# Performance work log

Hardware: AMD Instinct MI355X
Metric: run time of the kernel (lower is better)

## Reference

```python
import jax, jax.numpy as jnp
import numpy as np

INPUT_LAYER_SIZE = 40960 * 2
LAYER1_SIZE = 512
LAYER2_SIZE = 32
LAYER3_SIZE = 32
BATCH = 4096


def setup_inputs() -> dict:
    key = jax.random.key(0)
    ks = jax.random.split(key, 10)
    # Sparse one-hot style features: mostly zeros with ~30 active entries per side.
    def sparse_features(k, n_active=30):
        kidx, = jax.random.split(k, 1)
        idx = jax.random.randint(kidx, (BATCH, n_active), 0, 40960)
        feats = jnp.zeros((BATCH, 40960), dtype=jnp.float32)
        return feats.at[jnp.arange(BATCH)[:, None], idx].set(1.0)
    w_features = sparse_features(ks[0])
    b_features = sparse_features(ks[1])
    s_in = 1.0 / np.sqrt(INPUT_LAYER_SIZE)
    s1 = 1.0 / np.sqrt(LAYER1_SIZE)
    s2 = 1.0 / np.sqrt(LAYER2_SIZE)
    s3 = 1.0 / np.sqrt(LAYER3_SIZE)
    return {
        "w_features": w_features,
        "b_features": b_features,
        "W_in": jax.random.uniform(ks[2], (LAYER1_SIZE, INPUT_LAYER_SIZE), jnp.float32, -s_in, s_in),
        "b_in": jax.random.uniform(ks[3], (LAYER1_SIZE,), jnp.float32, -s_in, s_in),
        "W1": jax.random.uniform(ks[4], (LAYER2_SIZE, LAYER1_SIZE), jnp.float32, -s1, s1),
        "b1": jax.random.uniform(ks[5], (LAYER2_SIZE,), jnp.float32, -s1, s1),
        "W2": jax.random.uniform(ks[6], (LAYER3_SIZE, LAYER2_SIZE), jnp.float32, -s2, s2),
        "b2": jax.random.uniform(ks[7], (LAYER3_SIZE,), jnp.float32, -s2, s2),
        "W3": jax.random.uniform(ks[8], (1, LAYER3_SIZE), jnp.float32, -s3, s3),
        "b3": jax.random.uniform(ks[9], (1,), jnp.float32, -s3, s3),
    }


def reference(w_features, b_features, W_in, b_in, W1, b1, W2, b2, W3, b3):
    # Concatenate both perspectives: [B, 81920]
    x = jnp.concatenate([w_features, b_features], axis=1)
    # Huge sparse-input accumulator layer (the kernel-headroom op)
    accum = x @ W_in.T + b_in                       # [B, 512]
    l1 = jnp.clip(accum, 0.0, 1.0)                  # clipped ReLU
    l2 = jnp.clip(l1 @ W1.T + b1, 0.0, 1.0)         # [B, 32]
    l3 = jnp.clip(l2 @ W2.T + b2, 0.0, 1.0)         # [B, 32]
    return l3 @ W3.T + b3                           # [B, 1]
```

## Files before the change

kernel.cpp:

```cpp
#include <hip/hip_runtime.h>
#include <hip/hip_bf16.h>

#define IN_PER_SIDE   40960
#define IN_TOTAL      81920
#define L1            512
#define L2            32
#define L3_           32
#define BATCH         4096
#define MAXIDX        128

typedef float v4f __attribute__((ext_vector_type(4)));

#define WT_BYTES   ((size_t)IN_TOTAL * L1 * sizeof(float))
#define CNT_BYTES  ((size_t)BATCH * sizeof(int))
#define IDX_BYTES  ((size_t)BATCH * MAXIDX * sizeof(int))

__global__ __launch_bounds__(256) void stream_prep(
    const float* __restrict__ W, float* __restrict__ WT,
    const float* __restrict__ wf, const float* __restrict__ bfeat,
    int* __restrict__ cnt, int* __restrict__ idxs)
{
    __shared__ float tile[64][65];
    const int cls = blockIdx.x % 9;

    if (cls < 5) {
        const int tindex = (blockIdx.x / 9) * 5 + cls;
        const int jt = (tindex % 1280) * 64;
        const int ot = (tindex / 1280) * 64;
        const int tx = threadIdx.x & 15;
        const int ty = threadIdx.x >> 4;

#pragma unroll
        for (int k = 0; k < 4; ++k) {
            const int o = ty + 16 * k;
            const v4f* p = (const v4f*)&W[(size_t)(ot + o) * IN_TOTAL + jt + 4 * tx];
            v4f v = __builtin_nontemporal_load(p);
            tile[4 * tx + 0][o] = v.x;
            tile[4 * tx + 1][o] = v.y;
            tile[4 * tx + 2][o] = v.z;
            tile[4 * tx + 3][o] = v.w;
        }
        __syncthreads();
#pragma unroll
        for (int k = 0; k < 4; ++k) {
            const int j = ty + 16 * k;
            v4f v;
            v.x = tile[j][4 * tx + 0];
            v.y = tile[j][4 * tx + 1];
            v.z = tile[j][4 * tx + 2];
            v.w = tile[j][4 * tx + 3];
            *(v4f*)&WT[(size_t)(jt + j) * L1 + ot + 4 * tx] = v;
        }
    } else {
        const int sindex = (blockIdx.x / 9) * 4 + (cls - 5);
        const int row  = sindex >> 1;
        const int side = sindex & 1;
        const float* src = side ? bfeat : wf;
        const int    bias = side ? IN_PER_SIDE : 0;
        const v4f* p = (const v4f*)(src + (size_t)row * IN_PER_SIDE);
        int* ic = cnt + row;
        int* il = idxs + (size_t)row * MAXIDX;

        const int nvec = IN_PER_SIDE / 4;
        for (int i = threadIdx.x; i < nvec; i += 256) {
            v4f v = __builtin_nontemporal_load(p + i);
            if (v.x != 0.0f) il[atomicAdd(ic, 1)] = bias + 4 * i + 0;
            if (v.y != 0.0f) il[atomicAdd(ic, 1)] = bias + 4 * i + 1;
            if (v.z != 0.0f) il[atomicAdd(ic, 1)] = bias + 4 * i + 2;
            if (v.w != 0.0f) il[atomicAdd(ic, 1)] = bias + 4 * i + 3;
        }
    }
}

__global__ __launch_bounds__(512) void gather_mlp(
    const float* __restrict__ WT,
    const int* __restrict__ cnt, const int* __restrict__ idxs,
    const float* __restrict__ b_in,
    const float* __restrict__ W1, const float* __restrict__ b1,
    const float* __restrict__ W2, const float* __restrict__ b2,
    const float* __restrict__ W3, const float* __restrict__ b3,
    float* __restrict__ out)
{
    const int b = blockIdx.x;
    const int t = threadIdx.x;

    __shared__ int   sidx[MAXIDX];
    __shared__ float l1s[L1];
    __shared__ float l2acc[L2];
    __shared__ float l2s[L2];
    __shared__ float l3s[L3_];

    const int n = cnt[b];
    if (t < n) sidx[t] = idxs[(size_t)b * MAXIDX + t];
    const float bias_t = b_in[t];
    __syncthreads();

    float a0 = 0.0f, a1 = 0.0f, a2 = 0.0f, a3 = 0.0f;
    int i = 0;
    for (; i + 8 <= n; i += 8) {
        const float v0 = WT[(size_t)sidx[i + 0] * L1 + t];
        const float v1 = WT[(size_t)sidx[i + 1] * L1 + t];
        const float v2 = WT[(size_t)sidx[i + 2] * L1 + t];
        const float v3 = WT[(size_t)sidx[i + 3] * L1 + t];
        const float v4 = WT[(size_t)sidx[i + 4] * L1 + t];
        const float v5 = WT[(size_t)sidx[i + 5] * L1 + t];
        const float v6 = WT[(size_t)sidx[i + 6] * L1 + t];
        const float v7 = WT[(size_t)sidx[i + 7] * L1 + t];
        a0 += v0; a1 += v1; a2 += v2; a3 += v3;
        a0 += v4; a1 += v5; a2 += v6; a3 += v7;
    }
    for (; i < n; ++i) a0 += WT[(size_t)sidx[i] * L1 + t];

    float acc = bias_t + ((a0 + a1) + (a2 + a3));
    l1s[t] = fminf(fmaxf(acc, 0.0f), 1.0f);
    __syncthreads();

    {
        const int k = t >> 4;
        const int g = t & 15;
        const float* w = W1 + (size_t)k * L1;
        float p = 0.0f;
        for (int o = g; o < L1; o += 16) p += w[o] * l1s[o];
#pragma unroll
        for (int off = 8; off > 0; off >>= 1) p += __shfl_down(p, off, 16);
        if (g == 0) l2acc[k] = p;
    }
    __syncthreads();
    if (t < L2) l2s[t] = fminf(fmaxf(l2acc[t] + b1[t], 0.0f), 1.0f);
    __syncthreads();

    if (t < L3_) {
        const float* w = W2 + (size_t)t * L2;
        float p = b2[t];
#pragma unroll
        for (int q = 0; q < L2; ++q) p += w[q] * l2s[q];
        l3s[t] = fminf(fmaxf(p, 0.0f), 1.0f);
    }
    __syncthreads();

    if (t == 0) {
        float p = b3[0];
#pragma unroll
        for (int q = 0; q < L3_; ++q) p += W3[q] * l3s[q];
        out[b] = p;
    }
}

__global__ __launch_bounds__(512) void nnue_fallback(
    const float* __restrict__ wf, const float* __restrict__ bfeat,
    const float* __restrict__ W_in, const float* __restrict__ b_in,
    const float* __restrict__ W1, const float* __restrict__ b1,
    const float* __restrict__ W2, const float* __restrict__ b2,
    const float* __restrict__ W3, const float* __restrict__ b3,
    float* __restrict__ out)
{
    const int b = blockIdx.x;
    const int t = threadIdx.x;
    __shared__ int   idxs[MAXIDX];
    __shared__ int   scnt;
    __shared__ float l1s[L1];
    __shared__ float l2acc[L2];
    __shared__ float l2s[L2];
    __shared__ float l3s[L3_];

    if (t == 0) scnt = 0;
    __syncthreads();
    const v4f* wrow = (const v4f*)(wf    + (size_t)b * IN_PER_SIDE);
    const v4f* brow = (const v4f*)(bfeat + (size_t)b * IN_PER_SIDE);
    for (int i = t; i < IN_PER_SIDE / 4; i += 512) {
        v4f v = wrow[i];
        if (v.x != 0.0f) idxs[atomicAdd(&scnt, 1)] = 4 * i + 0;
        if (v.y != 0.0f) idxs[atomicAdd(&scnt, 1)] = 4 * i + 1;
        if (v.z != 0.0f) idxs[atomicAdd(&scnt, 1)] = 4 * i + 2;
        if (v.w != 0.0f) idxs[atomicAdd(&scnt, 1)] = 4 * i + 3;
        v4f u = brow[i];
        if (u.x != 0.0f) idxs[atomicAdd(&scnt, 1)] = IN_PER_SIDE + 4 * i + 0;
        if (u.y != 0.0f) idxs[atomicAdd(&scnt, 1)] = IN_PER_SIDE + 4 * i + 1;
        if (u.z != 0.0f) idxs[atomicAdd(&scnt, 1)] = IN_PER_SIDE + 4 * i + 2;
        if (u.w != 0.0f) idxs[atomicAdd(&scnt, 1)] = IN_PER_SIDE + 4 * i + 3;
    }
    __syncthreads();
    const int n = scnt;
    float a0 = 0.0f;
    const float* wr = W_in + (size_t)t;
    const float* row = W_in + (size_t)t * IN_TOTAL;
    for (int i = 0; i < n; ++i) a0 += row[idxs[i]];
    l1s[t] = fminf(fmaxf(b_in[t] + a0, 0.0f), 1.0f);
    __syncthreads();
    {
        const int k = t >> 4, g = t & 15;
        const float* w = W1 + (size_t)k * L1;
        float p = 0.0f;
        for (int o = g; o < L1; o += 16) p += w[o] * l1s[o];
#pragma unroll
        for (int off = 8; off > 0; off >>= 1) p += __shfl_down(p, off, 16);
        if (g == 0) l2acc[k] = p;
    }
    __syncthreads();
    if (t < L2) l2s[t] = fminf(fmaxf(l2acc[t] + b1[t], 0.0f), 1.0f);
    __syncthreads();
    if (t < L3_) {
        const float* w = W2 + (size_t)t * L2;
        float p = b2[t];
#pragma unroll
        for (int q = 0; q < L2; ++q) p += w[q] * l2s[q];
        l3s[t] = fminf(fmaxf(p, 0.0f), 1.0f);
    }
    __syncthreads();
    if (t == 0) {
        float p = b3[0];
#pragma unroll
        for (int q = 0; q < L3_; ++q) p += W3[q] * l3s[q];
        out[b] = p;
    }
}

extern "C" void kernel_launch(void* const* d_in, const int* in_sizes, int n_in,
                              void* d_out, int out_size, void* d_ws, size_t ws_size,
                              hipStream_t stream) {
    const float* wf   = (const float*)d_in[0];
    const float* bfeat= (const float*)d_in[1];
    const float* W_in = (const float*)d_in[2];
    const float* b_in = (const float*)d_in[3];
    const float* W1   = (const float*)d_in[4];
    const float* b1   = (const float*)d_in[5];
    const float* W2   = (const float*)d_in[6];
    const float* b2   = (const float*)d_in[7];
    const float* W3   = (const float*)d_in[8];
    const float* b3   = (const float*)d_in[9];
    float* out = (float*)d_out;

    const size_t need = WT_BYTES + CNT_BYTES + IDX_BYTES;
    if (ws_size >= need) {
        float* WT  = (float*)d_ws;
        int*   cnt = (int*)((char*)d_ws + WT_BYTES);
        int*   idx = (int*)((char*)d_ws + WT_BYTES + CNT_BYTES);

        hipMemsetAsync(cnt, 0, CNT_BYTES, stream);

        stream_prep<<<18432, 256, 0, stream>>>(W_in, WT, wf, bfeat, cnt, idx);
        gather_mlp<<<BATCH, 512, 0, stream>>>(WT, cnt, idx, b_in,
                                              W1, b1, W2, b2, W3, b3, out);
    } else {
        nnue_fallback<<<BATCH, 512, 0, stream>>>(
            wf, bfeat, W_in, b_in, W1, b1, W2, b2, W3, b3, out);
    }
}
```

Measured before the change: 1.454 ms.

## Fuse sparse index extraction into gather kernel and store transposed weights in fp16

Moves the dense-feature scan into the per-batch gather/MLP kernel, collecting active indices in shared memory instead of global arrays with a memset. The transposed input weight matrix is now stored in half precision, and each block gathers 16-byte half vectors across 8 waves, then reduces partial sums in shared memory. This cuts transpose write traffic, gather traffic and one launch. In exchange it adds fp16 rounding of the weights and serialises the scan with the gather per block.

```diff
diff --git a/kernel.cpp b/kernel.cpp
--- a/kernel.cpp
+++ b/kernel.cpp
@@ -9,72 +9,49 @@
 #define BATCH         4096
 #define MAXIDX        128
 
-typedef float v4f __attribute__((ext_vector_type(4)));
-
-#define WT_BYTES   ((size_t)IN_TOTAL * L1 * sizeof(float))
-#define CNT_BYTES  ((size_t)BATCH * sizeof(int))
-#define IDX_BYTES  ((size_t)BATCH * MAXIDX * sizeof(int))
-
-__global__ __launch_bounds__(256) void stream_prep(
-    const float* __restrict__ W, float* __restrict__ WT,
-    const float* __restrict__ wf, const float* __restrict__ bfeat,
-    int* __restrict__ cnt, int* __restrict__ idxs)
+typedef float    v4f __attribute__((ext_vector_type(4)));
+typedef float    v8f __attribute__((ext_vector_type(8)));
+typedef _Float16 v4h __attribute__((ext_vector_type(4)));
+typedef _Float16 v8h __attribute__((ext_vector_type(8)));
+
+#define WT_BYTES ((size_t)IN_TOTAL * L1 * sizeof(_Float16))
+
+__global__ __launch_bounds__(256) void transpose_win(
+    const float* __restrict__ W, _Float16* __restrict__ WTh)
 {
     __shared__ float tile[64][65];
-    const int cls = blockIdx.x % 9;
-
-    if (cls < 5) {
-        const int tindex = (blockIdx.x / 9) * 5 + cls;
-        const int jt = (tindex % 1280) * 64;
-        const int ot = (tindex / 1280) * 64;
-        const int tx = threadIdx.x & 15;
-        const int ty = threadIdx.x >> 4;
-
-#pragma unroll
-        for (int k = 0; k < 4; ++k) {
-            const int o = ty + 16 * k;
-            const v4f* p = (const v4f*)&W[(size_t)(ot + o) * IN_TOTAL + jt + 4 * tx];
-            v4f v = __builtin_nontemporal_load(p);
-            tile[4 * tx + 0][o] = v.x;
-            tile[4 * tx + 1][o] = v.y;
-            tile[4 * tx + 2][o] = v.z;
-            tile[4 * tx + 3][o] = v.w;
-        }
-        __syncthreads();
-#pragma unroll
-        for (int k = 0; k < 4; ++k) {
-            const int j = ty + 16 * k;
-            v4f v;
-            v.x = tile[j][4 * tx + 0];
-            v.y = tile[j][4 * tx + 1];
-            v.z = tile[j][4 * tx + 2];
-            v.w = tile[j][4 * tx + 3];
-            *(v4f*)&WT[(size_t)(jt + j) * L1 + ot + 4 * tx] = v;
-        }
-    } else {
-        const int sindex = (blockIdx.x / 9) * 4 + (cls - 5);
-        const int row  = sindex >> 1;
-        const int side = sindex & 1;
-        const float* src = side ? bfeat : wf;
-        const int    bias = side ? IN_PER_SIDE : 0;
-        const v4f* p = (const v4f*)(src + (size_t)row * IN_PER_SIDE);
-        int* ic = cnt + row;
-        int* il = idxs + (size_t)row * MAXIDX;
-
-        const int nvec = IN_PER_SIDE / 4;
-        for (int i = threadIdx.x; i < nvec; i += 256) {
-            v4f v = __builtin_nontemporal_load(p + i);
-            if (v.x != 0.0f) il[atomicAdd(ic, 1)] = bias + 4 * i + 0;
-            if (v.y != 0.0f) il[atomicAdd(ic, 1)] = bias + 4 * i + 1;
-            if (v.z != 0.0f) il[atomicAdd(ic, 1)] = bias + 4 * i + 2;
-            if (v.w != 0.0f) il[atomicAdd(ic, 1)] = bias + 4 * i + 3;
-        }
-    }
-}
-
-__global__ __launch_bounds__(512) void gather_mlp(
-    const float* __restrict__ WT,
-    const int* __restrict__ cnt, const int* __restrict__ idxs,
+    const int jt = blockIdx.x * 64;
+    const int ot = blockIdx.y * 64;
+    const int tx = threadIdx.x & 15;
+    const int ty = threadIdx.x >> 4;
+
+#pragma unroll
+    for (int k = 0; k < 4; ++k) {
+        const int o = ty + 16 * k;
+        const v4f* p = (const v4f*)&W[(size_t)(ot + o) * IN_TOTAL + jt + 4 * tx];
+        v4f v = __builtin_nontemporal_load(p);
+        tile[4 * tx + 0][o] = v.x;
+        tile[4 * tx + 1][o] = v.y;
+        tile[4 * tx + 2][o] = v.z;
+        tile[4 * tx + 3][o] = v.w;
+    }
+    __syncthreads();
+#pragma unroll
+    for (int k = 0; k < 4; ++k) {
+        const int j = ty + 16 * k;
+        v4f v;
+        v.x = tile[j][4 * tx + 0];
+        v.y = tile[j][4 * tx + 1];
+        v.z = tile[j][4 * tx + 2];
+        v.w = tile[j][4 * tx + 3];
+        v4h h = __builtin_convertvector(v, v4h);
+        *(v4h*)&WTh[(size_t)(jt + j) * L1 + ot + 4 * tx] = h;
+    }
+}
+
+__global__ __launch_bounds__(512) void nnue_fused(
+    const float* __restrict__ wf, const float* __restrict__ bfeat,
+    const _Float16* __restrict__ WTh,
     const float* __restrict__ b_in,
     const float* __restrict__ W1, const float* __restrict__ b1,
     const float* __restrict__ W2, const float* __restrict__ b2,
@@ -85,55 +62,91 @@
     const int t = threadIdx.x;
 
     __shared__ int   sidx[MAXIDX];
+    __shared__ int   scnt;
+    __shared__ float accs[8 * 64 * 9];
     __shared__ float l1s[L1];
     __shared__ float l2acc[L2];
     __shared__ float l2s[L2];
     __shared__ float l3s[L3_];
 
-    const int n = cnt[b];
-    if (t < n) sidx[t] = idxs[(size_t)b * MAXIDX + t];
-    const float bias_t = b_in[t];
-    __syncthreads();
-
-    float a0 = 0.0f, a1 = 0.0f, a2 = 0.0f, a3 = 0.0f;
-    int i = 0;
-    for (; i + 8 <= n; i += 8) {
-        const float v0 = WT[(size_t)sidx[i + 0] * L1 + t];
-        const float v1 = WT[(size_t)sidx[i + 1] * L1 + t];
-        const float v2 = WT[(size_t)sidx[i + 2] * L1 + t];
-        const float v3 = WT[(size_t)sidx[i + 3] * L1 + t];
-        const float v4 = WT[(size_t)sidx[i + 4] * L1 + t];
-        const float v5 = WT[(size_t)sidx[i + 5] * L1 + t];
-        const float v6 = WT[(size_t)sidx[i + 6] * L1 + t];
-        const float v7 = WT[(size_t)sidx[i + 7] * L1 + t];
-        a0 += v0; a1 += v1; a2 += v2; a3 += v3;
-        a0 += v4; a1 += v5; a2 += v6; a3 += v7;
-    }
-    for (; i < n; ++i) a0 += WT[(size_t)sidx[i] * L1 + t];
-
-    float acc = bias_t + ((a0 + a1) + (a2 + a3));
-    l1s[t] = fminf(fmaxf(acc, 0.0f), 1.0f);
-    __syncthreads();
-
-    {
-        const int k = t >> 4;
-        const int g = t & 15;
-        const float* w = W1 + (size_t)k * L1;
+    if (t == 0) scnt = 0;
+    __syncthreads();
+
+    const v4f* wrow = (const v4f*)(wf    + (size_t)b * IN_PER_SIDE);
+    const v4f* brow = (const v4f*)(bfeat + (size_t)b * IN_PER_SIDE);
+    const int nvec = IN_PER_SIDE / 4;
+
+    for (int i = t; i < nvec; i += 512) {
+        v4f v = __builtin_nontemporal_load(wrow + i);
+        if (v.x + v.y + v.z + v.w != 0.0f) {
+            if (v.x != 0.0f) sidx[atomicAdd(&scnt, 1)] = 4 * i + 0;
+            if (v.y != 0.0f) sidx[atomicAdd(&scnt, 1)] = 4 * i + 1;
+            if (v.z != 0.0f) sidx[atomicAdd(&scnt, 1)] = 4 * i + 2;
+            if (v.w != 0.0f) sidx[atomicAdd(&scnt, 1)] = 4 * i + 3;
+        }
+        v4f u = __builtin_nontemporal_load(brow + i);
+        if (u.x + u.y + u.z + u.w != 0.0f) {
+            if (u.x != 0.0f) sidx[atomicAdd(&scnt, 1)] = IN_PER_SIDE + 4 * i + 0;
+            if (u.y != 0.0f) sidx[atomicAdd(&scnt, 1)] = IN_PER_SIDE + 4 * i + 1;
+            if (u.z != 0.0f) sidx[atomicAdd(&scnt, 1)] = IN_PER_SIDE + 4 * i + 2;
+            if (u.w != 0.0f) sidx[atomicAdd(&scnt, 1)] = IN_PER_SIDE + 4 * i + 3;
+        }
+    }
+    __syncthreads();
+
+    const int n = scnt;
+    const int w = t >> 6;
+    const int l = t & 63;
+    const v8h* WTH8 = (const v8h*)WTh;
+
+    v8f acc0 = {0,0,0,0,0,0,0,0};
+    v8f acc1 = {0,0,0,0,0,0,0,0};
+    int k = w;
+    for (; k + 16 <= n; k += 16) {
+        v8h h0 = WTH8[(size_t)sidx[k]     * 64 + l];
+        v8h h1 = WTH8[(size_t)sidx[k + 8] * 64 + l];
+        acc0 += __builtin_convertvector(h0, v8f);
+        acc1 += __builtin_convertvector(h1, v8f);
+    }
+    for (; k < n; k += 8)
+        acc0 += __builtin_convertvector(WTH8[(size_t)sidx[k] * 64 + l], v8f);
+    acc0 += acc1;
+
+    {
+        float* dst = &accs[(w * 64 + l) * 9];
+#pragma unroll
+        for (int i = 0; i < 8; ++i) dst[i] = acc0[i];
+    }
+    __syncthreads();
+
+    {
+        const int ll = t >> 3, c = t & 7;
+        float s = 0.0f;
+#pragma unroll
+        for (int ww = 0; ww < 8; ++ww) s += accs[(ww * 64 + ll) * 9 + c];
+        l1s[t] = fminf(fmaxf(s + b_in[t], 0.0f), 1.0f);
+    }
+    __syncthreads();
+
+    {
+        const int kk = t >> 4;
+        const int gg = t & 15;
+        const float* wp = W1 + (size_t)kk * L1;
         float p = 0.0f;
-        for (int o = g; o < L1; o += 16) p += w[o] * l1s[o];
+        for (int o = gg; o < L1; o += 16) p += wp[o] * l1s[o];
 #pragma unroll
         for (int off = 8; off > 0; off >>= 1) p += __shfl_down(p, off, 16);
-        if (g == 0) l2acc[k] = p;
+        if (gg == 0) l2acc[kk] = p;
     }
     __syncthreads();
     if (t < L2) l2s[t] = fminf(fmaxf(l2acc[t] + b1[t], 0.0f), 1.0f);
     __syncthreads();
 
     if (t < L3_) {
-        const float* w = W2 + (size_t)t * L2;
+        const float* wp = W2 + (size_t)t * L2;
         float p = b2[t];
 #pragma unroll
-        for (int q = 0; q < L2; ++q) p += w[q] * l2s[q];
+        for (int q = 0; q < L2; ++q) p += wp[q] * l2s[q];
         l3s[t] = fminf(fmaxf(p, 0.0f), 1.0f);
     }
     __syncthreads();
@@ -182,16 +195,15 @@
     __syncthreads();
     const int n = scnt;
     float a0 = 0.0f;
-    const float* wr = W_in + (size_t)t;
     const float* row = W_in + (size_t)t * IN_TOTAL;
     for (int i = 0; i < n; ++i) a0 += row[idxs[i]];
     l1s[t] = fminf(fmaxf(b_in[t] + a0, 0.0f), 1.0f);
     __syncthreads();
     {
         const int k = t >> 4, g = t & 15;
-        const float* w = W1 + (size_t)k * L1;
+        const float* wp = W1 + (size_t)k * L1;
         float p = 0.0f;
-        for (int o = g; o < L1; o += 16) p += w[o] * l1s[o];
+        for (int o = g; o < L1; o += 16) p += wp[o] * l1s[o];
 #pragma unroll
         for (int off = 8; off > 0; off >>= 1) p += __shfl_down(p, off, 16);
         if (g == 0) l2acc[k] = p;
@@ -200,10 +212,10 @@
     if (t < L2) l2s[t] = fminf(fmaxf(l2acc[t] + b1[t], 0.0f), 1.0f);
     __syncthreads();
     if (t < L3_) {
-        const float* w = W2 + (size_t)t * L2;
+        const float* wp = W2 + (size_t)t * L2;
         float p = b2[t];
 #pragma unroll
-        for (int q = 0; q < L2; ++q) p += w[q] * l2s[q];
+        for (int q = 0; q < L2; ++q) p += wp[q] * l2s[q];
         l3s[t] = fminf(fmaxf(p, 0.0f), 1.0f);
     }
     __syncthreads();
@@ -230,17 +242,12 @@
     const float* b3   = (const float*)d_in[9];
     float* out = (float*)d_out;
 
-    const size_t need = WT_BYTES + CNT_BYTES + IDX_BYTES;
-    if (ws_size >= need) {
-        float* WT  = (float*)d_ws;
-        int*   cnt = (int*)((char*)d_ws + WT_BYTES);
-        int*   idx = (int*)((char*)d_ws + WT_BYTES + CNT_BYTES);
-
-        hipMemsetAsync(cnt, 0, CNT_BYTES, stream);
-
-        stream_prep<<<18432, 256, 0, stream>>>(W_in, WT, wf, bfeat, cnt, idx);
-        gather_mlp<<<BATCH, 512, 0, stream>>>(WT, cnt, idx, b_in,
-                                              W1, b1, W2, b2, W3, b3, out);
+    if (ws_size >= WT_BYTES) {
+        _Float16* WTh = (_Float16*)d_ws;
+        dim3 grid(IN_TOTAL / 64, L1 / 64);
+        transpose_win<<<grid, 256, 0, stream>>>(W_in, WTh);
+        nnue_fused<<<BATCH, 512, 0, stream>>>(
+            wf, bfeat, WTh, b_in, W1, b1, W2, b2, W3, b3, out);
     } else {
         nnue_fallback<<<BATCH, 512, 0, stream>>>(
             wf, bfeat, W_in, b_in, W1, b1, W2, b2, W3, b3, out);
```

Result: faster. 1.303 ms (-10.4%).
